# Performance work log

Hardware: AMD Instinct MI355X
Metric: run time of the kernel (lower is better)

## Reference

```python
import jax, jax.numpy as jnp
import numpy as np

# Module config (matches init_kwargs)
H, W = 512, 512          # in_dims
KH, KW = 32, 32          # kernel_dims
SH, SW = 16, 16          # stride
PH, PW = 8, 8            # padding
B = 64                   # batch
FULL_H, FULL_W = H + 2 * PH, W + 2 * PW            # 528, 528
NKH = 1 + (FULL_H - KH) // SH                      # 32
NKW = 1 + (FULL_W - KW) // SW                      # 32
NK = NKH * NKW                                     # 1024 output positions


def _patch_indices() -> np.ndarray:
    """Flat indices into the padded image for each sliding window.

    Reproduces the connectivity matrix columns of _create_connectivity_matrix:
    window k starts at (row*SH)*FULL_W + col*SW. Returns (NK, KH*KW) int32.
    """
    dr, dc = np.meshgrid(np.arange(KH), np.arange(KW), indexing="ij")
    off = (dr * FULL_W + dc).reshape(-1)                       # (KH*KW,)
    starts = (np.arange(NKH)[:, None] * SH * FULL_W
              + np.arange(NKW)[None, :] * SW).reshape(-1)      # (NK,)
    return (starts[:, None] + off[None, :]).astype(np.int32)


_IDX = jnp.asarray(_patch_indices())  # (NK, KH*KW), constant layout


def setup_inputs() -> dict:
    key = jax.random.key(0)
    kx, kw, kb = jax.random.split(key, 3)
    x = jax.random.normal(kx, (B, 1, H, W), dtype=jnp.float32)
    # Per-window weights = BSR values of the masked dense (padded_total, NK) matrix.
    # Xavier-normal scale of the underlying dense linear.
    std = float(np.sqrt(2.0 / (FULL_H * FULL_W + NK)))
    weight = jax.random.normal(kw, (NK, KH * KW), dtype=jnp.float32) * std
    bias = jax.random.normal(kb, (NK,), dtype=jnp.float32) * 0.01
    return {"x": x, "weight": weight, "bias": bias}


def reference(x, weight, bias):
    # x: (B, 1, H, W) -> pad -> flatten to (B, FULL_H*FULL_W)
    xp = jnp.pad(x, ((0, 0), (0, 0), (PH, PH), (PW, PW)))
    xf = xp.reshape(x.shape[0], FULL_H * FULL_W)
    # Gather the KHxKW window for every output position: (B, NK, KH*KW).
    patches = jnp.take(xf, _IDX, axis=1)
    # Untied locally-connected contraction (the block-sparse GEMM) + bias.
    out = jnp.einsum("bnk,nk->bn", patches, weight) + bias
    return out.reshape(x.shape[0], NKH, NKW)
```

## Files before the change

kernel.cpp:

```cpp
#include <hip/hip_runtime.h>

#define IMG_H 512
#define IMG_W 512
#define NKH 32
#define NKW 32
#define NK (NKH * NKW)
#define BATCH 64
#define NT 33

__global__ __launch_bounds__(256)
void bslc_tile_kernel(const float* __restrict__ x,
                      const float* __restrict__ w,
                      float* __restrict__ partial)
{
    const int tc = blockIdx.x;
    const int tr = blockIdx.y;
    const int bg = blockIdx.z;
    const int lane = threadIdx.x & 63;
    const int wv   = threadIdx.x >> 6;

    const int r  = lane >> 2;
    const int c0 = (lane & 3) * 4;

    float4 wreg[4];
#pragma unroll
    for (int q = 0; q < 4; ++q) {
        const int qr = q >> 1, qc = q & 1;
        const int nr = tr - qr, nc = tc - qc;
        if (nr >= 0 && nr < NKH && nc >= 0 && nc < NKW) {
            const size_t off = (size_t)(nr * NKW + nc) * 1024
                             + (size_t)(qr * 16 + r) * 32 + qc * 16 + c0;
            wreg[q] = *reinterpret_cast<const float4*>(w + off);
        } else {
            wreg[q] = make_float4(0.f, 0.f, 0.f, 0.f);
        }
    }

    const int rimg = tr * 16 - 8 + r;
    const int cimg = tc * 16 - 8 + c0;
    const bool interior = (tr >= 1) && (tr <= 31) && (tc >= 1) && (tc <= 31);
    const size_t xoff = (size_t)rimg * IMG_W + cimg;

#pragma unroll
    for (int i = 0; i < 8; ++i) {
        const int b = bg * 32 + wv + 4 * i;
        const float* xb = x + (size_t)b * (IMG_H * IMG_W);

        float4 xv;
        if (interior) {
            xv = *reinterpret_cast<const float4*>(xb + xoff);
        } else {
            xv = make_float4(0.f, 0.f, 0.f, 0.f);
            if (rimg >= 0 && rimg < IMG_H) {
#pragma unroll
                for (int e = 0; e < 4; ++e) {
                    const int c = cimg + e;
                    if (c >= 0 && c < IMG_W)
                        (&xv.x)[e] = xb[(size_t)rimg * IMG_W + c];
                }
            }
        }

        float s[4];
#pragma unroll
        for (int q = 0; q < 4; ++q) {
            float t;
            t = fmaf(xv.x, wreg[q].x, 0.f);
            t = fmaf(xv.y, wreg[q].y, t);
            t = fmaf(xv.z, wreg[q].z, t);
            t = fmaf(xv.w, wreg[q].w, t);
            s[q] = t;
        }

#pragma unroll
        for (int off = 32; off > 0; off >>= 1) {
#pragma unroll
            for (int q = 0; q < 4; ++q)
                s[q] += __shfl_xor(s[q], off, 64);
        }

        if (lane < 4) {
            const int qr = lane >> 1, qc = lane & 1;
            const int nr = tr - qr, nc = tc - qc;
            if (nr >= 0 && nr < NKH && nc >= 0 && nc < NKW) {
                const float sv = (lane == 0) ? s[0]
                               : (lane == 1) ? s[1]
                               : (lane == 2) ? s[2] : s[3];
                partial[((size_t)b * NK + (nr * NKW + nc)) * 4 + lane] = sv;
            }
        }
    }
}

__global__ __launch_bounds__(256)
void bslc_reduce_kernel(const float* __restrict__ partial,
                        const float* __restrict__ bias,
                        float* __restrict__ out)
{
    const int idx = blockIdx.x * 256 + threadIdx.x;
    const int n = idx & (NK - 1);
    const float4 p = reinterpret_cast<const float4*>(partial)[idx];
    out[idx] = p.x + p.y + p.z + p.w + bias[n];
}

extern "C" void kernel_launch(void* const* d_in, const int* in_sizes, int n_in,
                              void* d_out, int out_size, void* d_ws, size_t ws_size,
                              hipStream_t stream) {
    const float* x    = (const float*)d_in[0];
    const float* wgt  = (const float*)d_in[1];
    const float* bias = (const float*)d_in[2];
    float* out        = (float*)d_out;
    float* partial    = (float*)d_ws;

    dim3 grid1(NT, NT, 2);
    bslc_tile_kernel<<<grid1, 256, 0, stream>>>(x, wgt, partial);

    dim3 grid2((BATCH * NK) / 256);
    bslc_reduce_kernel<<<grid2, 256, 0, stream>>>(partial, bias, out);
}
```

Measured before the change: 118.2 us.

## Stage input tiles for all batches in shared memory, assign batch per lane

The tile kernel now loads the 16x16 input tile for all 64 batch images into a skewed LDS buffer, then each wave takes one quadrant and each lane one batch, accumulating a dot product over the tile without cross-lane shuffle reductions. The partial layout becomes [quadrant][position][batch], and the reduce kernel sums the four quadrants and writes the output transposed. This removes the per-batch wavefront shuffle reductions and the batch split across grid z, at the cost of 64KB of LDS per block, a barrier, halved block count, and weight loads that are uniform per wave but repeated from global memory.

```diff
diff --git a/kernel.cpp b/kernel.cpp
--- a/kernel.cpp
+++ b/kernel.cpp
@@ -13,82 +13,70 @@
                       const float* __restrict__ w,
                       float* __restrict__ partial)
 {
+    __shared__ float4 xt[64][64];
     const int tc = blockIdx.x;
     const int tr = blockIdx.y;
-    const int bg = blockIdx.z;
-    const int lane = threadIdx.x & 63;
-    const int wv   = threadIdx.x >> 6;
+    const int t  = threadIdx.x;
+    const int lane = t & 63;
+    const int wv   = t >> 6;
 
-    const int r  = lane >> 2;
-    const int c0 = (lane & 3) * 4;
+    const int kc = lane;
+    const int r  = kc >> 2;
+    const int c4 = kc & 3;
+    const int rimg = tr * 16 - 8 + r;
+    const int cimg = tc * 16 - 8 + c4 * 4;
+    const bool interior = (tr >= 1) & (tr <= 31) & (tc >= 1) & (tc <= 31);
+    const size_t xoff = (size_t)rimg * IMG_W + cimg;
+    const int col = (0 + kc) & 63;
 
-    float4 wreg[4];
+    if (interior) {
 #pragma unroll
-    for (int q = 0; q < 4; ++q) {
-        const int qr = q >> 1, qc = q & 1;
-        const int nr = tr - qr, nc = tc - qc;
-        if (nr >= 0 && nr < NKH && nc >= 0 && nc < NKW) {
-            const size_t off = (size_t)(nr * NKW + nc) * 1024
-                             + (size_t)(qr * 16 + r) * 32 + qc * 16 + c0;
-            wreg[q] = *reinterpret_cast<const float4*>(w + off);
-        } else {
-            wreg[q] = make_float4(0.f, 0.f, 0.f, 0.f);
+        for (int i = 0; i < 16; ++i) {
+            const int b = wv + 4 * i;
+            const float4 xv = *reinterpret_cast<const float4*>(
+                x + (size_t)b * (IMG_H * IMG_W) + xoff);
+            xt[kc][(b + kc) & 63] = xv;
         }
-    }
-
-    const int rimg = tr * 16 - 8 + r;
-    const int cimg = tc * 16 - 8 + c0;
-    const bool interior = (tr >= 1) && (tr <= 31) && (tc >= 1) && (tc <= 31);
-    const size_t xoff = (size_t)rimg * IMG_W + cimg;
-
+    } else {
 #pragma unroll
-    for (int i = 0; i < 8; ++i) {
-        const int b = bg * 32 + wv + 4 * i;
-        const float* xb = x + (size_t)b * (IMG_H * IMG_W);
-
-        float4 xv;
-        if (interior) {
-            xv = *reinterpret_cast<const float4*>(xb + xoff);
-        } else {
-            xv = make_float4(0.f, 0.f, 0.f, 0.f);
+        for (int i = 0; i < 16; ++i) {
+            const int b = wv + 4 * i;
+            float4 xv = make_float4(0.f, 0.f, 0.f, 0.f);
             if (rimg >= 0 && rimg < IMG_H) {
+                const float* xb = x + (size_t)b * (IMG_H * IMG_W)
+                                + (size_t)rimg * IMG_W;
 #pragma unroll
                 for (int e = 0; e < 4; ++e) {
                     const int c = cimg + e;
-                    if (c >= 0 && c < IMG_W)
-                        (&xv.x)[e] = xb[(size_t)rimg * IMG_W + c];
+                    if (c >= 0 && c < IMG_W) (&xv.x)[e] = xb[c];
                 }
             }
+            xt[kc][(b + kc) & 63] = xv;
         }
+    }
+    (void)col;
+    __syncthreads();
 
-        float s[4];
+    const int q  = __builtin_amdgcn_readfirstlane(wv);
+    const int qr = q >> 1, qc = q & 1;
+    const int nr = tr - qr, nc = tc - qc;
+    if (nr >= 0 && nr < NKH && nc >= 0 && nc < NKW) {
+        const int n = nr * NKW + nc;
+        const float* wq = w + (size_t)n * 1024 + (size_t)(qr * 16) * 32 + qc * 16;
+        const int b = lane;
+
+        float s0 = 0.f, s1 = 0.f, s2 = 0.f, s3 = 0.f;
 #pragma unroll
-        for (int q = 0; q < 4; ++q) {
-            float t;
-            t = fmaf(xv.x, wreg[q].x, 0.f);
-            t = fmaf(xv.y, wreg[q].y, t);
-            t = fmaf(xv.z, wreg[q].z, t);
-            t = fmaf(xv.w, wreg[q].w, t);
-            s[q] = t;
+        for (int kk = 0; kk < 64; ++kk) {
+            const float4 xv = xt[kk][(b + kk) & 63];
+            const float4 wv4 = *reinterpret_cast<const float4*>(
+                wq + (kk >> 2) * 32 + (kk & 3) * 4);
+            s0 = fmaf(xv.x, wv4.x, s0);
+            s1 = fmaf(xv.y, wv4.y, s1);
+            s2 = fmaf(xv.z, wv4.z, s2);
+            s3 = fmaf(xv.w, wv4.w, s3);
         }
-
-#pragma unroll
-        for (int off = 32; off > 0; off >>= 1) {
-#pragma unroll
-            for (int q = 0; q < 4; ++q)
-                s[q] += __shfl_xor(s[q], off, 64);
-        }
-
-        if (lane < 4) {
-            const int qr = lane >> 1, qc = lane & 1;
-            const int nr = tr - qr, nc = tc - qc;
-            if (nr >= 0 && nr < NKH && nc >= 0 && nc < NKW) {
-                const float sv = (lane == 0) ? s[0]
-                               : (lane == 1) ? s[1]
-                               : (lane == 2) ? s[2] : s[3];
-                partial[((size_t)b * NK + (nr * NKW + nc)) * 4 + lane] = sv;
-            }
-        }
+        partial[((size_t)q * NK + n) * 64 + b] = (s0 + s1) + (s2 + s3);
     }
 }
 
@@ -97,10 +85,14 @@
                         const float* __restrict__ bias,
                         float* __restrict__ out)
 {
-    const int idx = blockIdx.x * 256 + threadIdx.x;
-    const int n = idx & (NK - 1);
-    const float4 p = reinterpret_cast<const float4*>(partial)[idx];
-    out[idx] = p.x + p.y + p.z + p.w + bias[n];
+    const int g = blockIdx.x * 256 + threadIdx.x;
+    const int n = g >> 6;
+    const int b = g & 63;
+    float s = bias[n];
+#pragma unroll
+    for (int q = 0; q < 4; ++q)
+        s += partial[((size_t)q * NK + n) * 64 + b];
+    out[(size_t)b * NK + n] = s;
 }
 
 extern "C" void kernel_launch(void* const* d_in, const int* in_sizes, int n_in,
@@ -112,7 +104,7 @@
     float* out        = (float*)d_out;
     float* partial    = (float*)d_ws;
 
-    dim3 grid1(NT, NT, 2);
+    dim3 grid1(NT, NT);
     bslc_tile_kernel<<<grid1, 256, 0, stream>>>(x, wgt, partial);
 
     dim3 grid2((BATCH * NK) / 256);
```

Result: slower. 122.3 us (+3.4%).
